# Kernel optimization log

Measured on AMD Instinct MI355X. Metric: run time of the kernel, lower is better.

## Reference

```python
import jax, jax.numpy as jnp
import numpy as np

D = 1024      # in_features
H = 768       # hidden_features per routed expert
E = 8         # n_routed_experts
K = 2         # n_activated_experts
NS = 2        # n_shared_experts
ROUTE_SCALE = 1.0


def setup_inputs() -> dict:
    key = jax.random.key(0)
    ks = jax.random.split(key, 6)
    s = 0.02
    return {
        "x": jax.random.normal(ks[0], (2, 1024, D), jnp.float32),
        "gate_w": jax.random.normal(ks[1], (E, D), jnp.float32) * s,
        "W1": jax.random.normal(ks[2], (E, 2 * H, D), jnp.float32) * s,   # expert fc1 (y|gate)
        "W2": jax.random.normal(ks[3], (E, D, H), jnp.float32) * s,       # expert fc2
        "Ws1": jax.random.normal(ks[4], (2 * NS * H, D), jnp.float32) * s,  # shared fc1
        "Ws2": jax.random.normal(ks[5], (D, NS * H), jnp.float32) * s,      # shared fc2
    }


def _gated_mlp(x, w1, w2):
    # GatedMLP: fc1 -> chunk(2) -> y * silu(gate) -> fc2, all bias-free
    h = x @ w1.T
    y, g = jnp.split(h, 2, axis=-1)
    return (y * jax.nn.silu(g)) @ w2.T


def reference(x, gate_w, W1, W2, Ws1, Ws2):
    x_shape = x.shape
    xf = x.reshape(-1, D)                 # [T, D]
    T = xf.shape[0]

    # --- Gate: softmax scores in fp32, top-k routing ---
    scores = jax.nn.softmax((xf @ gate_w.T).astype(jnp.float32), axis=-1)  # [T, E]
    top_vals, top_idx = jax.lax.top_k(scores, K)
    # no bias branch (in_features != 7168): gathered original scores == top_k values
    weights = (top_vals * ROUTE_SCALE).astype(x.dtype)                      # [T, K]

    # Dense per-token/expert combine weights (0 for unselected experts);
    # mathematically identical to the per-expert gather/scatter-add combine.
    w_dense = jnp.zeros((T, E), x.dtype).at[jnp.arange(T)[:, None], top_idx].set(weights)

    # --- Routed experts (stacked GatedMLPs) ---
    h = jnp.einsum('td,ehd->teh', xf, W1)        # [T, E, 2H]
    y, g = jnp.split(h, 2, axis=-1)
    eo = jnp.einsum('teh,edh->ted', y * jax.nn.silu(g), W2)  # [T, E, D]
    z = jnp.einsum('te,ted->td', w_dense, eo)    # weighted combine

    # --- Shared experts ---
    z = z + _gated_mlp(xf, Ws1, Ws2)
    return z.reshape(x_shape)
```

## Files before the change

### kernel.cpp

```cpp
#include <hip/hip_runtime.h>
#include <hip/hip_bf16.h>


typedef short bf16x8 __attribute__((ext_vector_type(8)));
typedef float f32x4 __attribute__((ext_vector_type(4)));

__device__ __forceinline__ unsigned short f2b(float f) {
    __hip_bfloat16 h = __float2bfloat16(f);
    return *reinterpret_cast<unsigned short*>(&h);
}

__device__ __forceinline__ void ldst16(const unsigned short* g, unsigned short* l) {
    __builtin_amdgcn_global_load_lds(
        (const __attribute__((address_space(1))) unsigned int*)g,
        (__attribute__((address_space(3))) unsigned int*)l, 16, 0, 0);
}

__device__ __forceinline__ void cvt8(const float* s, unsigned short* d, int j) {
    const float4* sp = reinterpret_cast<const float4*>(s) + (size_t)j * 2;
    float4 v0 = sp[0], v1 = sp[1];
    union { unsigned short u[8]; uint4 v; } o;
    o.u[0]=f2b(v0.x); o.u[1]=f2b(v0.y); o.u[2]=f2b(v0.z); o.u[3]=f2b(v0.w);
    o.u[4]=f2b(v1.x); o.u[5]=f2b(v1.y); o.u[6]=f2b(v1.z); o.u[7]=f2b(v1.w);
    *(reinterpret_cast<uint4*>(d) + j) = o.v;
}

__global__ __launch_bounds__(256) void k_conv(const float* __restrict__ x,
                                              const float* __restrict__ W1,
                                              const float* __restrict__ Ws1,
                                              const float* __restrict__ W2,
                                              const float* __restrict__ Ws2,
                                              unsigned short* __restrict__ xb,
                                              unsigned short* __restrict__ W1b,
                                              unsigned short* __restrict__ Ws1b,
                                              unsigned short* __restrict__ W2b,
                                              unsigned short* __restrict__ Ws2b) {
    int i = blockIdx.x * 256 + threadIdx.x;
    if (i < 262144)        cvt8(x,   xb,   i);
    else if (i < 1835008)  cvt8(W1,  W1b,  i - 262144);
    else if (i < 2228224)  cvt8(Ws1, Ws1b, i - 1835008);
    else if (i < 3014656)  cvt8(W2,  W2b,  i - 2228224);
    else if (i < 3211264)  cvt8(Ws2, Ws2b, i - 3014656);
}

__global__ __launch_bounds__(256) void k_gate(const float* __restrict__ x,
                                              const float* __restrict__ gw,
                                              int* __restrict__ topk_e,
                                              float* __restrict__ topk_w) {
    int t = blockIdx.x;
    int lane = threadIdx.x & 63, w = threadIdx.x >> 6;
    __shared__ float sc[8];
    const float* xr = x + (size_t)t * 1024;
    for (int e = w; e < 8; e += 4) {
        const float* g = gw + (size_t)e * 1024;
        float s = 0.f;
        for (int k = lane; k < 1024; k += 64) s += xr[k] * g[k];
        for (int off = 32; off > 0; off >>= 1) s += __shfl_down(s, off, 64);
        if (lane == 0) sc[e] = s;
    }
    __syncthreads();
    if (threadIdx.x == 0) {
        float m = sc[0];
        for (int e = 1; e < 8; e++) m = fmaxf(m, sc[e]);
        float ex[8], sum = 0.f;
        for (int e = 0; e < 8; e++) { ex[e] = expf(sc[e] - m); sum += ex[e]; }
        float inv = 1.f / sum;
        int i1 = 0;
        for (int e = 1; e < 8; e++) if (sc[e] > sc[i1]) i1 = e;
        int i2 = -1; float s2 = -1e30f;
        for (int e = 0; e < 8; e++) if (e != i1 && sc[e] > s2) { s2 = sc[e]; i2 = e; }
        topk_e[t * 2]     = i1; topk_w[t * 2]     = ex[i1] * inv;
        topk_e[t * 2 + 1] = i2; topk_w[t * 2 + 1] = ex[i2] * inv;
    }
}

__global__ __launch_bounds__(256) void k_sort(const int* __restrict__ topk_e,
                                              const float* __restrict__ topk_w,
                                              int* __restrict__ tokslot,
                                              float* __restrict__ wroute,
                                              int* __restrict__ cnt) {
    __shared__ int lcnt[8], lcur[8];
    int tid = threadIdx.x;
    if (tid < 8) { lcnt[tid] = 0; lcur[tid] = 0; }
    __syncthreads();
    for (int i = tid; i < 4096; i += 256) atomicAdd(&lcnt[topk_e[i]], 1);
    __syncthreads();
    if (tid < 8) cnt[tid] = lcnt[tid];
    for (int i = tid; i < 4096; i += 256) {
        int e = topk_e[i];
        int pos = atomicAdd(&lcur[e], 1);
        tokslot[e * 2048 + pos] = i;
        wroute[e * 2048 + pos]  = topk_w[i];
    }
}

__global__ __launch_bounds__(256) void k_fc1u(const unsigned short* __restrict__ xb,
                                              const unsigned short* __restrict__ W1b,
                                              const unsigned short* __restrict__ Ws1b,
                                              const int* __restrict__ tokslot,
                                              const float* __restrict__ wroute,
                                              const int* __restrict__ cnt,
                                              unsigned short* __restrict__ act_r,
                                              unsigned short* __restrict__ act_s) {
    __shared__ alignas(16) unsigned short As[64 * 64];
    __shared__ alignas(16) unsigned short Bs[128 * 64];
    const int tid = threadIdx.x, lane = tid & 63, w = tid >> 6;
    const int wr = w >> 1, wc = w & 1;
    const int bid = blockIdx.x;

    int routed, e = 0, m0, h0, gOff, Te;
    const unsigned short* Bp;
    if (bid < 864) {
        int ht = bid % 12, mt = bid / 12;
        int pre = 0, sel = -1, base = 0;
        for (int ee = 0; ee < 8; ee++) {
            int til = (cnt[ee] + 63) >> 6;
            if (sel < 0 && mt < pre + til) { sel = ee; base = pre; }
            pre += til;
        }
        if (sel < 0) return;
        routed = 1; e = sel; m0 = (mt - base) * 64; h0 = ht * 64;
        Bp = W1b + (size_t)e * 1536 * 1024; gOff = 768; Te = cnt[e];
    } else {
        int sid = bid - 864;
        routed = 0; m0 = (sid / 24) * 64; h0 = (sid % 24) * 64;
        Bp = Ws1b; gOff = 1536; Te = 2048;
    }

    const int arow0 = tid >> 3, arow1 = 32 + (tid >> 3);
    const int kc = tid & 7;
    const int kA0 = (kc ^ (arow0 & 7)) * 8;
    const int kA1 = (kc ^ (arow1 & 7)) * 8;
    int t0, t1;
    if (routed) {
        t0 = (m0 + arow0 < Te) ? (tokslot[e * 2048 + m0 + arow0] >> 1) : 0;
        t1 = (m0 + arow1 < Te) ? (tokslot[e * 2048 + m0 + arow1] >> 1) : 0;
    } else { t0 = m0 + arow0; t1 = m0 + arow1; }

    size_t bsrc[4]; int bkof[4];
    for (int q = 0; q < 4; q++) {
        int row = q * 32 + (tid >> 3);
        int grow = (row < 64) ? (h0 + row) : (gOff + h0 + row - 64);
        bsrc[q] = (size_t)grow * 1024;
        bkof[q] = (kc ^ (row & 7)) * 8;
    }

    f32x4 accy[2][2], accg[2][2];
    for (int i = 0; i < 2; i++)
        for (int j = 0; j < 2; j++) {
            accy[i][j] = (f32x4){0.f, 0.f, 0.f, 0.f};
            accg[i][j] = (f32x4){0.f, 0.f, 0.f, 0.f};
        }

    for (int k0 = 0; k0 < 1024; k0 += 64) {
        ldst16(xb + (size_t)t0 * 1024 + k0 + kA0, As + tid * 8);
        ldst16(xb + (size_t)t1 * 1024 + k0 + kA1, As + (256 + tid) * 8);
        for (int q = 0; q < 4; q++)
            ldst16(Bp + bsrc[q] + k0 + bkof[q], Bs + (q * 256 + tid) * 8);
        __syncthreads();
        for (int kh = 0; kh < 2; kh++) {
            const int cq = kh * 4 + (lane >> 4);
            bf16x8 a[2], by[2], bg[2];
            for (int i = 0; i < 2; i++) {
                int r = 32 * wr + 16 * i + (lane & 15);
                a[i] = *(const bf16x8*)&As[r * 64 + ((cq ^ (r & 7)) << 3)];
            }
            for (int j = 0; j < 2; j++) {
                int ry = 32 * wc + 16 * j + (lane & 15);
                by[j] = *(const bf16x8*)&Bs[ry * 64 + ((cq ^ (ry & 7)) << 3)];
                int rg = 64 + ry;
                bg[j] = *(const bf16x8*)&Bs[rg * 64 + ((cq ^ (rg & 7)) << 3)];
            }
            for (int i = 0; i < 2; i++)
                for (int j = 0; j < 2; j++) {
                    accy[i][j] = __builtin_amdgcn_mfma_f32_16x16x32_bf16(a[i], by[j], accy[i][j], 0, 0, 0);
                    accg[i][j] = __builtin_amdgcn_mfma_f32_16x16x32_bf16(a[i], bg[j], accg[i][j], 0, 0, 0);
                }
        }
        __syncthreads();
    }

    for (int i = 0; i < 2; i++)
        for (int r = 0; r < 4; r++) {
            int irow = m0 + 32 * wr + 16 * i + ((lane >> 4) << 2) + r;
            if (irow >= Te) continue;
            float sw = routed ? wroute[e * 2048 + irow] : 1.0f;
            for (int j = 0; j < 2; j++) {
                float y = accy[i][j][r], g = accg[i][j][r];
                float sg = g / (1.0f + __expf(-g));
                int col = h0 + 32 * wc + 16 * j + (lane & 15);
                if (routed)
                    act_r[((size_t)e * 2048 + irow) * 768 + col] = f2b(sw * y * sg);
                else
                    act_s[(size_t)irow * 1536 + col] = f2b(y * sg);
            }
        }
}

__global__ __launch_bounds__(256) void k_fc2s(const unsigned short* __restrict__ act_s,
                                              const unsigned short* __restrict__ Ws2b,
                                              float* __restrict__ out) {
    __shared__ alignas(16) unsigned short As[64 * 64];
    __shared__ alignas(16) unsigned short Bs[64 * 64];
    const int m0 = blockIdx.x * 64, n0 = blockIdx.y * 64;
    const int tid = threadIdx.x, lane = tid & 63, w = tid >> 6;
    const int wr = w >> 1, wc = w & 1;
    const int kc = tid & 7;

    size_t asrc[2], bsrc[2]; int kof[2];
    for (int q = 0; q < 2; q++) {
        int row = q * 32 + (tid >> 3);
        kof[q] = (kc ^ (row & 7)) * 8;
        asrc[q] = (size_t)(m0 + row) * 1536;
        bsrc[q] = (size_t)(n0 + row) * 1536;
    }

    f32x4 acc[2][2];
    for (int i = 0; i < 2; i++)
        for (int j = 0; j < 2; j++) acc[i][j] = (f32x4){0.f, 0.f, 0.f, 0.f};

    for (int k0 = 0; k0 < 1536; k0 += 64) {
        for (int q = 0; q < 2; q++) {
            ldst16(act_s + asrc[q] + k0 + kof[q], As + (q * 256 + tid) * 8);
            ldst16(Ws2b  + bsrc[q] + k0 + kof[q], Bs + (q * 256 + tid) * 8);
        }
        __syncthreads();
        for (int kh = 0; kh < 2; kh++) {
            const int cq = kh * 4 + (lane >> 4);
            bf16x8 a[2], b[2];
            for (int i = 0; i < 2; i++) {
                int r = 32 * wr + 16 * i + (lane & 15);
                a[i] = *(const bf16x8*)&As[r * 64 + ((cq ^ (r & 7)) << 3)];
            }
            for (int j = 0; j < 2; j++) {
                int r = 32 * wc + 16 * j + (lane & 15);
                b[j] = *(const bf16x8*)&Bs[r * 64 + ((cq ^ (r & 7)) << 3)];
            }
            for (int i = 0; i < 2; i++)
                for (int j = 0; j < 2; j++)
                    acc[i][j] = __builtin_amdgcn_mfma_f32_16x16x32_bf16(a[i], b[j], acc[i][j], 0, 0, 0);
        }
        __syncthreads();
    }

    for (int i = 0; i < 2; i++)
        for (int r = 0; r < 4; r++) {
            int t = m0 + 32 * wr + 16 * i + ((lane >> 4) << 2) + r;
            for (int j = 0; j < 2; j++) {
                int col = n0 + 32 * wc + 16 * j + (lane & 15);
                out[(size_t)t * 1024 + col] = acc[i][j][r];
            }
        }
}

__global__ __launch_bounds__(256) void k_fc2r(const unsigned short* __restrict__ act_r,
                                              const unsigned short* __restrict__ W2b,
                                              const int* __restrict__ tokslot,
                                              const int* __restrict__ cnt,
                                              float* __restrict__ out) {
    __shared__ alignas(16) unsigned short As[64 * 64];
    __shared__ alignas(16) unsigned short Bs[64 * 64];
    const int tid = threadIdx.x, lane = tid & 63, w = tid >> 6;
    const int wr = w >> 1, wc = w & 1;
    const int nt = blockIdx.x & 15, mt = blockIdx.x >> 4;

    int pre = 0, sel = -1, base = 0;
    for (int ee = 0; ee < 8; ee++) {
        int til = (cnt[ee] + 63) >> 6;
        if (sel < 0 && mt < pre + til) { sel = ee; base = pre; }
        pre += til;
    }
    if (sel < 0) return;
    const int e = sel, m0 = (mt - base) * 64, n0 = nt * 64;
    const int Te = cnt[e];
    const unsigned short* Ab = act_r + (size_t)e * 2048 * 768;
    const unsigned short* Bb = W2b + (size_t)e * 1024 * 768;
    const int kc = tid & 7;

    size_t asrc[2], bsrc[2]; int kof[2];
    for (int q = 0; q < 2; q++) {
        int row = q * 32 + (tid >> 3);
        kof[q] = (kc ^ (row & 7)) * 8;
        asrc[q] = (size_t)(m0 + row) * 768;
        bsrc[q] = (size_t)(n0 + row) * 768;
    }

    f32x4 acc[2][2];
    for (int i = 0; i < 2; i++)
        for (int j = 0; j < 2; j++) acc[i][j] = (f32x4){0.f, 0.f, 0.f, 0.f};

    for (int k0 = 0; k0 < 768; k0 += 64) {
        for (int q = 0; q < 2; q++) {
            ldst16(Ab + asrc[q] + k0 + kof[q], As + (q * 256 + tid) * 8);
            ldst16(Bb + bsrc[q] + k0 + kof[q], Bs + (q * 256 + tid) * 8);
        }
        __syncthreads();
        for (int kh = 0; kh < 2; kh++) {
            const int cq = kh * 4 + (lane >> 4);
            bf16x8 a[2], b[2];
            for (int i = 0; i < 2; i++) {
                int r = 32 * wr + 16 * i + (lane & 15);
                a[i] = *(const bf16x8*)&As[r * 64 + ((cq ^ (r & 7)) << 3)];
            }
            for (int j = 0; j < 2; j++) {
                int r = 32 * wc + 16 * j + (lane & 15);
                b[j] = *(const bf16x8*)&Bs[r * 64 + ((cq ^ (r & 7)) << 3)];
            }
            for (int i = 0; i < 2; i++)
                for (int j = 0; j < 2; j++)
                    acc[i][j] = __builtin_amdgcn_mfma_f32_16x16x32_bf16(a[i], b[j], acc[i][j], 0, 0, 0);
        }
        __syncthreads();
    }

    for (int i = 0; i < 2; i++)
        for (int r = 0; r < 4; r++) {
            int irow = m0 + 32 * wr + 16 * i + ((lane >> 4) << 2) + r;
            if (irow >= Te) continue;
            int t = tokslot[e * 2048 + irow] >> 1;
            for (int j = 0; j < 2; j++) {
                int col = n0 + 32 * wc + 16 * j + (lane & 15);
                atomicAdd(out + (size_t)t * 1024 + col, acc[i][j][r]);
            }
        }
}

extern "C" void kernel_launch(void* const* d_in, const int* in_sizes, int n_in,
                              void* d_out, int out_size, void* d_ws, size_t ws_size,
                              hipStream_t stream) {
    const float* x   = (const float*)d_in[0];
    const float* gw  = (const float*)d_in[1];
    const float* W1  = (const float*)d_in[2];
    const float* W2  = (const float*)d_in[3];
    const float* Ws1 = (const float*)d_in[4];
    const float* Ws2 = (const float*)d_in[5];
    float* out = (float*)d_out;

    char* ws = (char*)d_ws;
    unsigned short* xb    = (unsigned short*)(ws + 0);
    unsigned short* W1b   = (unsigned short*)(ws + 4194304);
    unsigned short* Ws1b  = (unsigned short*)(ws + 29360128);
    unsigned short* W2b   = (unsigned short*)(ws + 35651584);
    unsigned short* Ws2b  = (unsigned short*)(ws + 48234496);
    unsigned short* act_r = (unsigned short*)(ws + 51380224);
    unsigned short* act_s = (unsigned short*)(ws + 76546048);
    int*            topk_e  = (int*)(ws + 82837504);
    float*          topk_w  = (float*)(ws + 82853888);
    int*            tokslot = (int*)(ws + 82870272);
    float*          wroute  = (float*)(ws + 82935808);
    int*            cnt     = (int*)(ws + 83001344);

    k_conv<<<12544, 256, 0, stream>>>(x, W1, Ws1, W2, Ws2, xb, W1b, Ws1b, W2b, Ws2b);
    k_gate<<<2048, 256, 0, stream>>>(x, gw, topk_e, topk_w);
    k_sort<<<1, 256, 0, stream>>>(topk_e, topk_w, tokslot, wroute, cnt);
    k_fc1u<<<1632, 256, 0, stream>>>(xb, W1b, Ws1b, tokslot, wroute, cnt, act_r, act_s);
    k_fc2s<<<dim3(32, 16), 256, 0, stream>>>(act_s, Ws2b, out);
    k_fc2r<<<1152, 256, 0, stream>>>(act_r, W2b, tokslot, cnt, out);
}
```

Measured before the change: 250.7 us.

## Treat shared experts as pseudo-experts, enlarge GEMM tiles, fuse x conversion into gate

```diff
diff --git a/kernel.cpp b/kernel.cpp
--- a/kernel.cpp
+++ b/kernel.cpp
@@ -25,41 +25,50 @@
     *(reinterpret_cast<uint4*>(d) + j) = o.v;
 }
 
-__global__ __launch_bounds__(256) void k_conv(const float* __restrict__ x,
-                                              const float* __restrict__ W1,
+__global__ __launch_bounds__(256) void k_conv(const float* __restrict__ W1,
                                               const float* __restrict__ Ws1,
                                               const float* __restrict__ W2,
                                               const float* __restrict__ Ws2,
-                                              unsigned short* __restrict__ xb,
                                               unsigned short* __restrict__ W1b,
                                               unsigned short* __restrict__ Ws1b,
                                               unsigned short* __restrict__ W2b,
                                               unsigned short* __restrict__ Ws2b) {
     int i = blockIdx.x * 256 + threadIdx.x;
-    if (i < 262144)        cvt8(x,   xb,   i);
-    else if (i < 1835008)  cvt8(W1,  W1b,  i - 262144);
-    else if (i < 2228224)  cvt8(Ws1, Ws1b, i - 1835008);
-    else if (i < 3014656)  cvt8(W2,  W2b,  i - 2228224);
-    else if (i < 3211264)  cvt8(Ws2, Ws2b, i - 3014656);
+    if (i < 1572864)       cvt8(W1,  W1b,  i);
+    else if (i < 1966080)  cvt8(Ws1, Ws1b, i - 1572864);
+    else if (i < 2752512)  cvt8(W2,  W2b,  i - 1966080);
+    else if (i < 2949120)  cvt8(Ws2, Ws2b, i - 2752512);
 }
 
 __global__ __launch_bounds__(256) void k_gate(const float* __restrict__ x,
                                               const float* __restrict__ gw,
+                                              unsigned short* __restrict__ xb,
                                               int* __restrict__ topk_e,
-                                              float* __restrict__ topk_w) {
-    int t = blockIdx.x;
-    int lane = threadIdx.x & 63, w = threadIdx.x >> 6;
+                                              float* __restrict__ topk_w,
+                                              float* __restrict__ out) {
+    const int t = blockIdx.x, tid = threadIdx.x;
+    const int lane = tid & 63, w = tid >> 6;
+    __shared__ float red[4][8];
     __shared__ float sc[8];
-    const float* xr = x + (size_t)t * 1024;
-    for (int e = w; e < 8; e += 4) {
-        const float* g = gw + (size_t)e * 1024;
-        float s = 0.f;
-        for (int k = lane; k < 1024; k += 64) s += xr[k] * g[k];
-        for (int off = 32; off > 0; off >>= 1) s += __shfl_down(s, off, 64);
-        if (lane == 0) sc[e] = s;
-    }
+
+    float4 v = reinterpret_cast<const float4*>(x + (size_t)t * 1024)[tid];
+    union { unsigned short u[4]; ushort2 h2[2]; } o;
+    o.u[0]=f2b(v.x); o.u[1]=f2b(v.y); o.u[2]=f2b(v.z); o.u[3]=f2b(v.w);
+    reinterpret_cast<ushort4*>(xb + (size_t)t * 1024)[tid] = *(ushort4*)o.u;
+
+    float p[8];
+    for (int e = 0; e < 8; e++) {
+        float4 g = reinterpret_cast<const float4*>(gw + (size_t)e * 1024)[tid];
+        p[e] = v.x*g.x + v.y*g.y + v.z*g.z + v.w*g.w;
+    }
+    for (int e = 0; e < 8; e++)
+        for (int off = 32; off > 0; off >>= 1) p[e] += __shfl_down(p[e], off, 64);
+    if (lane == 0)
+        for (int e = 0; e < 8; e++) red[w][e] = p[e];
     __syncthreads();
-    if (threadIdx.x == 0) {
+    if (tid < 8) sc[tid] = red[0][tid] + red[1][tid] + red[2][tid] + red[3][tid];
+    __syncthreads();
+    if (tid == 0) {
         float m = sc[0];
         for (int e = 1; e < 8; e++) m = fmaxf(m, sc[e]);
         float ex[8], sum = 0.f;
@@ -72,6 +81,7 @@
         topk_e[t * 2]     = i1; topk_w[t * 2]     = ex[i1] * inv;
         topk_e[t * 2 + 1] = i2; topk_w[t * 2 + 1] = ex[i2] * inv;
     }
+    reinterpret_cast<float4*>(out + (size_t)t * 1024)[tid] = (float4){0.f, 0.f, 0.f, 0.f};
 }
 
 __global__ __launch_bounds__(256) void k_sort(const int* __restrict__ topk_e,
@@ -92,6 +102,10 @@
         tokslot[e * 2048 + pos] = i;
         wroute[e * 2048 + pos]  = topk_w[i];
     }
+    for (int i = tid; i < 2048; i += 256) {
+        tokslot[8 * 2048 + i] = i << 1;  wroute[8 * 2048 + i] = 1.0f;
+        tokslot[9 * 2048 + i] = i << 1;  wroute[9 * 2048 + i] = 1.0f;
+    }
 }
 
 __global__ __launch_bounds__(256) void k_fc1u(const unsigned short* __restrict__ xb,
@@ -100,226 +114,157 @@
                                               const int* __restrict__ tokslot,
                                               const float* __restrict__ wroute,
                                               const int* __restrict__ cnt,
-                                              unsigned short* __restrict__ act_r,
-                                              unsigned short* __restrict__ act_s) {
-    __shared__ alignas(16) unsigned short As[64 * 64];
+                                              unsigned short* __restrict__ act) {
+    __shared__ alignas(16) unsigned short As[128 * 64];
+    __shared__ alignas(16) unsigned short Bs[256 * 64];
+    const int tid = threadIdx.x, lane = tid & 63, w = tid >> 6;
+    const int wr = w >> 1, wc = w & 1;
+    const int mt = blockIdx.x / 6, ht = blockIdx.x % 6;
+
+    int pre = 0, sel = -1, base = 0;
+    for (int ee = 0; ee < 10; ee++) {
+        int til = (ee < 8) ? ((cnt[ee] + 127) >> 7) : 16;
+        if (sel < 0 && mt < pre + til) { sel = ee; base = pre; }
+        pre += til;
+    }
+    if (sel < 0) return;
+    const int e = sel, m0 = (mt - base) * 128, h0 = ht * 128;
+    const int Te = (e < 8) ? cnt[e] : 2048;
+    const unsigned short* Bp = (e < 8) ? (W1b + (size_t)e * 1536 * 1024)
+                                       : (Ws1b + (size_t)(e - 8) * 768 * 1024);
+    const int gOff = (e < 8) ? 768 : 1536;
+
+    const int kc = tid & 7;
+    int aoff[4], boff[8];
+    for (int q = 0; q < 4; q++) {
+        int row = q * 32 + (tid >> 3);
+        int idx = m0 + row;
+        int tk = (idx < Te) ? (tokslot[e * 2048 + idx] >> 1) : 0;
+        aoff[q] = tk * 1024 + ((kc ^ (row & 7)) << 3);
+    }
+    for (int q = 0; q < 8; q++) {
+        int row = q * 32 + (tid >> 3);
+        int grow = (row < 128) ? (h0 + row) : (gOff + h0 + row - 128);
+        boff[q] = grow * 1024 + ((kc ^ (row & 7)) << 3);
+    }
+
+    f32x4 accy[4][4], accg[4][4];
+    for (int i = 0; i < 4; i++)
+        for (int j = 0; j < 4; j++) {
+            accy[i][j] = (f32x4){0.f, 0.f, 0.f, 0.f};
+            accg[i][j] = (f32x4){0.f, 0.f, 0.f, 0.f};
+        }
+
+    for (int k0 = 0; k0 < 1024; k0 += 64) {
+        for (int q = 0; q < 4; q++) ldst16(xb + aoff[q] + k0, As + (q * 256 + tid) * 8);
+        for (int q = 0; q < 8; q++) ldst16(Bp + boff[q] + k0, Bs + (q * 256 + tid) * 8);
+        __syncthreads();
+        for (int kh = 0; kh < 2; kh++) {
+            const int cq = kh * 4 + (lane >> 4);
+            bf16x8 a[4], by[4], bg[4];
+            for (int i = 0; i < 4; i++) {
+                int r = 64 * wr + 16 * i + (lane & 15);
+                a[i] = *(const bf16x8*)&As[r * 64 + ((cq ^ (r & 7)) << 3)];
+            }
+            for (int j = 0; j < 4; j++) {
+                int r = 64 * wc + 16 * j + (lane & 15);
+                by[j] = *(const bf16x8*)&Bs[r * 64 + ((cq ^ (r & 7)) << 3)];
+                int rg = 128 + r;
+                bg[j] = *(const bf16x8*)&Bs[rg * 64 + ((cq ^ (rg & 7)) << 3)];
+            }
+            for (int i = 0; i < 4; i++)
+                for (int j = 0; j < 4; j++) {
+                    accy[i][j] = __builtin_amdgcn_mfma_f32_16x16x32_bf16(a[i], by[j], accy[i][j], 0, 0, 0);
+                    accg[i][j] = __builtin_amdgcn_mfma_f32_16x16x32_bf16(a[i], bg[j], accg[i][j], 0, 0, 0);
+                }
+        }
+        __syncthreads();
+    }
+
+    for (int i = 0; i < 4; i++)
+        for (int r = 0; r < 4; r++) {
+            int irow = m0 + 64 * wr + 16 * i + ((lane >> 4) << 2) + r;
+            if (irow >= Te) continue;
+            float sw = wroute[e * 2048 + irow];
+            for (int j = 0; j < 4; j++) {
+                float y = accy[i][j][r], g = accg[i][j][r];
+                float sg = g / (1.0f + __expf(-g));
+                int col = h0 + 64 * wc + 16 * j + (lane & 15);
+                act[((size_t)e * 2048 + irow) * 768 + col] = f2b(sw * y * sg);
+            }
+        }
+}
+
+__global__ __launch_bounds__(256) void k_fc2u(const unsigned short* __restrict__ act,
+                                              const unsigned short* __restrict__ W2b,
+                                              const unsigned short* __restrict__ Ws2b,
+                                              const int* __restrict__ tokslot,
+                                              const int* __restrict__ cnt,
+                                              float* __restrict__ out) {
+    __shared__ alignas(16) unsigned short As[128 * 64];
     __shared__ alignas(16) unsigned short Bs[128 * 64];
     const int tid = threadIdx.x, lane = tid & 63, w = tid >> 6;
     const int wr = w >> 1, wc = w & 1;
-    const int bid = blockIdx.x;
-
-    int routed, e = 0, m0, h0, gOff, Te;
-    const unsigned short* Bp;
-    if (bid < 864) {
-        int ht = bid % 12, mt = bid / 12;
-        int pre = 0, sel = -1, base = 0;
-        for (int ee = 0; ee < 8; ee++) {
-            int til = (cnt[ee] + 63) >> 6;
-            if (sel < 0 && mt < pre + til) { sel = ee; base = pre; }
-            pre += til;
-        }
-        if (sel < 0) return;
-        routed = 1; e = sel; m0 = (mt - base) * 64; h0 = ht * 64;
-        Bp = W1b + (size_t)e * 1536 * 1024; gOff = 768; Te = cnt[e];
-    } else {
-        int sid = bid - 864;
-        routed = 0; m0 = (sid / 24) * 64; h0 = (sid % 24) * 64;
-        Bp = Ws1b; gOff = 1536; Te = 2048;
-    }
-
-    const int arow0 = tid >> 3, arow1 = 32 + (tid >> 3);
+    const int mt = blockIdx.x >> 3, nt = blockIdx.x & 7;
+
+    int pre = 0, sel = -1, base = 0;
+    for (int ee = 0; ee < 10; ee++) {
+        int til = (ee < 8) ? ((cnt[ee] + 127) >> 7) : 16;
+        if (sel < 0 && mt < pre + til) { sel = ee; base = pre; }
+        pre += til;
+    }
+    if (sel < 0) return;
+    const int e = sel, m0 = (mt - base) * 128, n0 = nt * 128;
+    const int Te = (e < 8) ? cnt[e] : 2048;
+    const unsigned short* Ab = act + (size_t)e * 2048 * 768;
+    const unsigned short* Bb = (e < 8) ? (W2b + (size_t)e * 1024 * 768)
+                                       : (Ws2b + (size_t)(e - 8) * 768);
+    const int bstride = (e < 8) ? 768 : 1536;
+
     const int kc = tid & 7;
-    const int kA0 = (kc ^ (arow0 & 7)) * 8;
-    const int kA1 = (kc ^ (arow1 & 7)) * 8;
-    int t0, t1;
-    if (routed) {
-        t0 = (m0 + arow0 < Te) ? (tokslot[e * 2048 + m0 + arow0] >> 1) : 0;
-        t1 = (m0 + arow1 < Te) ? (tokslot[e * 2048 + m0 + arow1] >> 1) : 0;
-    } else { t0 = m0 + arow0; t1 = m0 + arow1; }
-
-    size_t bsrc[4]; int bkof[4];
+    int aoff[4], boff[4];
     for (int q = 0; q < 4; q++) {
         int row = q * 32 + (tid >> 3);
-        int grow = (row < 64) ? (h0 + row) : (gOff + h0 + row - 64);
-        bsrc[q] = (size_t)grow * 1024;
-        bkof[q] = (kc ^ (row & 7)) * 8;
-    }
-
-    f32x4 accy[2][2], accg[2][2];
-    for (int i = 0; i < 2; i++)
-        for (int j = 0; j < 2; j++) {
-            accy[i][j] = (f32x4){0.f, 0.f, 0.f, 0.f};
-            accg[i][j] = (f32x4){0.f, 0.f, 0.f, 0.f};
-        }
-
-    for (int k0 = 0; k0 < 1024; k0 += 64) {
-        ldst16(xb + (size_t)t0 * 1024 + k0 + kA0, As + tid * 8);
-        ldst16(xb + (size_t)t1 * 1024 + k0 + kA1, As + (256 + tid) * 8);
-        for (int q = 0; q < 4; q++)
-            ldst16(Bp + bsrc[q] + k0 + bkof[q], Bs + (q * 256 + tid) * 8);
+        int ko = (kc ^ (row & 7)) << 3;
+        aoff[q] = (m0 + row) * 768 + ko;
+        boff[q] = (n0 + row) * bstride + ko;
+    }
+
+    f32x4 acc[4][4];
+    for (int i = 0; i < 4; i++)
+        for (int j = 0; j < 4; j++) acc[i][j] = (f32x4){0.f, 0.f, 0.f, 0.f};
+
+    for (int k0 = 0; k0 < 768; k0 += 64) {
+        for (int q = 0; q < 4; q++) {
+            ldst16(Ab + aoff[q] + k0, As + (q * 256 + tid) * 8);
+            ldst16(Bb + boff[q] + k0, Bs + (q * 256 + tid) * 8);
+        }
         __syncthreads();
         for (int kh = 0; kh < 2; kh++) {
             const int cq = kh * 4 + (lane >> 4);
-            bf16x8 a[2], by[2], bg[2];
-            for (int i = 0; i < 2; i++) {
-                int r = 32 * wr + 16 * i + (lane & 15);
+            bf16x8 a[4], b[4];
+            for (int i = 0; i < 4; i++) {
+                int r = 64 * wr + 16 * i + (lane & 15);
                 a[i] = *(const bf16x8*)&As[r * 64 + ((cq ^ (r & 7)) << 3)];
             }
-            for (int j = 0; j < 2; j++) {
-                int ry = 32 * wc + 16 * j + (lane & 15);
-                by[j] = *(const bf16x8*)&Bs[ry * 64 + ((cq ^ (ry & 7)) << 3)];
-                int rg = 64 + ry;
-                bg[j] = *(const bf16x8*)&Bs[rg * 64 + ((cq ^ (rg & 7)) << 3)];
-            }
-            for (int i = 0; i < 2; i++)
-                for (int j = 0; j < 2; j++) {
-                    accy[i][j] = __builtin_amdgcn_mfma_f32_16x16x32_bf16(a[i], by[j], accy[i][j], 0, 0, 0);
-                    accg[i][j] = __builtin_amdgcn_mfma_f32_16x16x32_bf16(a[i], bg[j], accg[i][j], 0, 0, 0);
-                }
+            for (int j = 0; j < 4; j++) {
+                int r = 64 * wc + 16 * j + (lane & 15);
+                b[j] = *(const bf16x8*)&Bs[r * 64 + ((cq ^ (r & 7)) << 3)];
+            }
+            for (int i = 0; i < 4; i++)
+                for (int j = 0; j < 4; j++)
+                    acc[i][j] = __builtin_amdgcn_mfma_f32_16x16x32_bf16(a[i], b[j], acc[i][j], 0, 0, 0);
         }
         __syncthreads();
     }
 
-    for (int i = 0; i < 2; i++)
+    for (int i = 0; i < 4; i++)
         for (int r = 0; r < 4; r++) {
-            int irow = m0 + 32 * wr + 16 * i + ((lane >> 4) << 2) + r;
-            if (irow >= Te) continue;
-            float sw = routed ? wroute[e * 2048 + irow] : 1.0f;
-            for (int j = 0; j < 2; j++) {
-                float y = accy[i][j][r], g = accg[i][j][r];
-                float sg = g / (1.0f + __expf(-g));
-                int col = h0 + 32 * wc + 16 * j + (lane & 15);
-                if (routed)
-                    act_r[((size_t)e * 2048 + irow) * 768 + col] = f2b(sw * y * sg);
-                else
-                    act_s[(size_t)irow * 1536 + col] = f2b(y * sg);
-            }
-        }
-}
-
-__global__ __launch_bounds__(256) void k_fc2s(const unsigned short* __restrict__ act_s,
-                                              const unsigned short* __restrict__ Ws2b,
-                                              float* __restrict__ out) {
-    __shared__ alignas(16) unsigned short As[64 * 64];
-    __shared__ alignas(16) unsigned short Bs[64 * 64];
-    const int m0 = blockIdx.x * 64, n0 = blockIdx.y * 64;
-    const int tid = threadIdx.x, lane = tid & 63, w = tid >> 6;
-    const int wr = w >> 1, wc = w & 1;
-    const int kc = tid & 7;
-
-    size_t asrc[2], bsrc[2]; int kof[2];
-    for (int q = 0; q < 2; q++) {
-        int row = q * 32 + (tid >> 3);
-        kof[q] = (kc ^ (row & 7)) * 8;
-        asrc[q] = (size_t)(m0 + row) * 1536;
-        bsrc[q] = (size_t)(n0 + row) * 1536;
-    }
-
-    f32x4 acc[2][2];
-    for (int i = 0; i < 2; i++)
-        for (int j = 0; j < 2; j++) acc[i][j] = (f32x4){0.f, 0.f, 0.f, 0.f};
-
-    for (int k0 = 0; k0 < 1536; k0 += 64) {
-        for (int q = 0; q < 2; q++) {
-            ldst16(act_s + asrc[q] + k0 + kof[q], As + (q * 256 + tid) * 8);
-            ldst16(Ws2b  + bsrc[q] + k0 + kof[q], Bs + (q * 256 + tid) * 8);
-        }
-        __syncthreads();
-        for (int kh = 0; kh < 2; kh++) {
-            const int cq = kh * 4 + (lane >> 4);
-            bf16x8 a[2], b[2];
-            for (int i = 0; i < 2; i++) {
-                int r = 32 * wr + 16 * i + (lane & 15);
-                a[i] = *(const bf16x8*)&As[r * 64 + ((cq ^ (r & 7)) << 3)];
-            }
-            for (int j = 0; j < 2; j++) {
-                int r = 32 * wc + 16 * j + (lane & 15);
-                b[j] = *(const bf16x8*)&Bs[r * 64 + ((cq ^ (r & 7)) << 3)];
-            }
-            for (int i = 0; i < 2; i++)
-                for (int j = 0; j < 2; j++)
-                    acc[i][j] = __builtin_amdgcn_mfma_f32_16x16x32_bf16(a[i], b[j], acc[i][j], 0, 0, 0);
-        }
-        __syncthreads();
-    }
-
-    for (int i = 0; i < 2; i++)
-        for (int r = 0; r < 4; r++) {
-            int t = m0 + 32 * wr + 16 * i + ((lane >> 4) << 2) + r;
-            for (int j = 0; j < 2; j++) {
-                int col = n0 + 32 * wc + 16 * j + (lane & 15);
-                out[(size_t)t * 1024 + col] = acc[i][j][r];
-            }
-        }
-}
-
-__global__ __launch_bounds__(256) void k_fc2r(const unsigned short* __restrict__ act_r,
-                                              const unsigned short* __restrict__ W2b,
-                                              const int* __restrict__ tokslot,
-                                              const int* __restrict__ cnt,
-                                              float* __restrict__ out) {
-    __shared__ alignas(16) unsigned short As[64 * 64];
-    __shared__ alignas(16) unsigned short Bs[64 * 64];
-    const int tid = threadIdx.x, lane = tid & 63, w = tid >> 6;
-    const int wr = w >> 1, wc = w & 1;
-    const int nt = blockIdx.x & 15, mt = blockIdx.x >> 4;
-
-    int pre = 0, sel = -1, base = 0;
-    for (int ee = 0; ee < 8; ee++) {
-        int til = (cnt[ee] + 63) >> 6;
-        if (sel < 0 && mt < pre + til) { sel = ee; base = pre; }
-        pre += til;
-    }
-    if (sel < 0) return;
-    const int e = sel, m0 = (mt - base) * 64, n0 = nt * 64;
-    const int Te = cnt[e];
-    const unsigned short* Ab = act_r + (size_t)e * 2048 * 768;
-    const unsigned short* Bb = W2b + (size_t)e * 1024 * 768;
-    const int kc = tid & 7;
-
-    size_t asrc[2], bsrc[2]; int kof[2];
-    for (int q = 0; q < 2; q++) {
-        int row = q * 32 + (tid >> 3);
-        kof[q] = (kc ^ (row & 7)) * 8;
-        asrc[q] = (size_t)(m0 + row) * 768;
-        bsrc[q] = (size_t)(n0 + row) * 768;
-    }
-
-    f32x4 acc[2][2];
-    for (int i = 0; i < 2; i++)
-        for (int j = 0; j < 2; j++) acc[i][j] = (f32x4){0.f, 0.f, 0.f, 0.f};
-
-    for (int k0 = 0; k0 < 768; k0 += 64) {
-        for (int q = 0; q < 2; q++) {
-            ldst16(Ab + asrc[q] + k0 + kof[q], As + (q * 256 + tid) * 8);
-            ldst16(Bb + bsrc[q] + k0 + kof[q], Bs + (q * 256 + tid) * 8);
-        }
-        __syncthreads();
-        for (int kh = 0; kh < 2; kh++) {
-            const int cq = kh * 4 + (lane >> 4);
-            bf16x8 a[2], b[2];
-            for (int i = 0; i < 2; i++) {
-                int r = 32 * wr + 16 * i + (lane & 15);
-                a[i] = *(const bf16x8*)&As[r * 64 + ((cq ^ (r & 7)) << 3)];
-            }
-            for (int j = 0; j < 2; j++) {
-                int r = 32 * wc + 16 * j + (lane & 15);
-                b[j] = *(const bf16x8*)&Bs[r * 64 + ((cq ^ (r & 7)) << 3)];
-            }
-            for (int i = 0; i < 2; i++)
-                for (int j = 0; j < 2; j++)
-                    acc[i][j] = __builtin_amdgcn_mfma_f32_16x16x32_bf16(a[i], b[j], acc[i][j], 0, 0, 0);
-        }
-        __syncthreads();
-    }
-
-    for (int i = 0; i < 2; i++)
-        for (int r = 0; r < 4; r++) {
-            int irow = m0 + 32 * wr + 16 * i + ((lane >> 4) << 2) + r;
+            int irow = m0 + 64 * wr + 16 * i + ((lane >> 4) << 2) + r;
             if (irow >= Te) continue;
             int t = tokslot[e * 2048 + irow] >> 1;
-            for (int j = 0; j < 2; j++) {
-                int col = n0 + 32 * wc + 16 * j + (lane & 15);
+            for (int j = 0; j < 4; j++) {
+                int col = n0 + 64 * wc + 16 * j + (lane & 15);
                 atomicAdd(out + (size_t)t * 1024 + col, acc[i][j][r]);
             }
         }
@@ -342,18 +287,16 @@
     unsigned short* Ws1b  = (unsigned short*)(ws + 29360128);
     unsigned short* W2b   = (unsigned short*)(ws + 35651584);
     unsigned short* Ws2b  = (unsigned short*)(ws + 48234496);
-    unsigned short* act_r = (unsigned short*)(ws + 51380224);
-    unsigned short* act_s = (unsigned short*)(ws + 76546048);
+    unsigned short* act   = (unsigned short*)(ws + 51380224);
     int*            topk_e  = (int*)(ws + 82837504);
     float*          topk_w  = (float*)(ws + 82853888);
     int*            tokslot = (int*)(ws + 82870272);
-    float*          wroute  = (float*)(ws + 82935808);
-    int*            cnt     = (int*)(ws + 83001344);
-
-    k_conv<<<12544, 256, 0, stream>>>(x, W1, Ws1, W2, Ws2, xb, W1b, Ws1b, W2b, Ws2b);
-    k_gate<<<2048, 256, 0, stream>>>(x, gw, topk_e, topk_w);
+    float*          wroute  = (float*)(ws + 82952192);
+    int*            cnt     = (int*)(ws + 83034112);
+
+    k_conv<<<11520, 256, 0, stream>>>(W1, Ws1, W2, Ws2, W1b, Ws1b, W2b, Ws2b);
+    k_gate<<<2048, 256, 0, stream>>>(x, gw, xb, topk_e, topk_w, out);
     k_sort<<<1, 256, 0, stream>>>(topk_e, topk_w, tokslot, wroute, cnt);
-    k_fc1u<<<1632, 256, 0, stream>>>(xb, W1b, Ws1b, tokslot, wroute, cnt, act_r, act_s);
-    k_fc2s<<<dim3(32, 16), 256, 0, stream>>>(act_s, Ws2b, out);
-    k_fc2r<<<1152, 256, 0, stream>>>(act_r, W2b, tokslot, cnt, out);
-}
+    k_fc1u<<<426, 256, 0, stream>>>(xb, W1b, Ws1b, tokslot, wroute, cnt, act);
+    k_fc2u<<<568, 256, 0, stream>>>(act, W2b, Ws2b, tokslot, cnt, out);
+}
```

Result: slower. 265.3 us (+5.8%).
